# Performance work log

Hardware: AMD Instinct MI355X
Metric: run time of the kernel (lower is better)

The kernel has to match this reference:

```python
import jax, jax.numpy as jnp
import numpy as np

N_DRUG, N_TARGET, N_EDGES, H = 50000, 20000, 500000, 256


def setup_inputs() -> dict:
    key = jax.random.key(0)
    ks = jax.random.split(key, 6)
    s = 1.0 / np.sqrt(2 * H)
    return {
        "z_drug": jax.random.normal(ks[0], (N_DRUG, H), dtype=jnp.float32),
        "z_target": jax.random.normal(ks[1], (N_TARGET, H), dtype=jnp.float32),
        "row": jax.random.randint(ks[2], (N_EDGES,), 0, N_DRUG, dtype=jnp.int64),
        "col": jax.random.randint(ks[3], (N_EDGES,), 0, N_TARGET, dtype=jnp.int64),
        "W1": jax.random.normal(ks[4], (2 * H, H), dtype=jnp.float32) * s,
        "b1": jnp.zeros((H,), dtype=jnp.float32),
        "W2": jax.random.normal(ks[5], (H, 1), dtype=jnp.float32) * (1.0 / np.sqrt(H)),
        "b2": jnp.zeros((1,), dtype=jnp.float32),
    }


def reference(z_drug, z_target, row, col, W1, b1, W2, b2):
    # gather endpoint embeddings by edge index, concat -> [E, 2H]
    zc = jnp.concatenate([z_drug[row], z_target[col]], axis=-1)
    h = jax.nn.relu(zc @ W1 + b1)          # [E, H]
    return h @ W2 + b2                     # [E, 1]
```

## Files before the change

### kernel.cpp

```cpp
#include <hip/hip_runtime.h>
#include <hip/hip_bf16.h>
#include <stdint.h>


typedef unsigned short u16;
typedef __attribute__((ext_vector_type(8))) short short8;
typedef __attribute__((ext_vector_type(4))) float f32x4;

#define HDIM 256
#define KDIM 512
#define BM 64
#define BK 64
#define NWAVE 4

__device__ __forceinline__ u16 f2bf(float f) {
  union { float f; uint32_t u; } v; v.f = f;
  uint32_t u = v.u;
  return (u16)((u + 0x7fffu + ((u >> 16) & 1u)) >> 16);
}

__device__ __forceinline__ void gl2lds16(const void* g, void* l) {
  __builtin_amdgcn_global_load_lds(
      (const __attribute__((address_space(1))) unsigned int*)g,
      (__attribute__((address_space(3))) unsigned int*)l,
      16, 0, 0);
}

__global__ void cvt_bf16_kernel(const float* __restrict__ src,
                                u16* __restrict__ dst, int n4) {
  int i = blockIdx.x * blockDim.x + threadIdx.x;
  if (i >= n4) return;
  float4 v = ((const float4*)src)[i];
  ushort4 o;
  o.x = f2bf(v.x); o.y = f2bf(v.y); o.z = f2bf(v.z); o.w = f2bf(v.w);
  ((ushort4*)dst)[i] = o;
}

__global__ void w1t_kernel(const float* __restrict__ w1, u16* __restrict__ w1t) {
  int t = blockIdx.x * blockDim.x + threadIdx.x;
  int n = t >> 9, k = t & 511;
  w1t[n * 512 + k] = f2bf(w1[k * 256 + n]);
}

__global__ __launch_bounds__(256, 2) void edge_mlp_kernel(
    const u16* __restrict__ zd, const u16* __restrict__ zt,
    const int* __restrict__ row, const int* __restrict__ col,
    const u16* __restrict__ w1t, const float* __restrict__ b1,
    const float* __restrict__ w2, const float* __restrict__ b2,
    float* __restrict__ out, int E) {
  __shared__ u16 lA[BM * BK];
  __shared__ u16 lB[HDIM * BK];
  __shared__ float lP[NWAVE * BM];

  const int tid  = threadIdx.x;
  const int wid  = tid >> 6;
  const int lane = tid & 63;
  const int e0   = blockIdx.x * BM;

  const int eA = wid * 16 + (lane >> 3);
  const int g1 = min(e0 + eA, E - 1);
  const int g2 = min(e0 + eA + 8, E - 1);
  const int slog = ((lane & 7) ^ ((lane >> 3) & 7)) * 8;

  const u16* pD1 = zd + (size_t)row[g1] * HDIM + slog;
  const u16* pT1 = zt + (size_t)col[g1] * HDIM + slog;
  const u16* pD2 = zd + (size_t)row[g2] * HDIM + slog;
  const u16* pT2 = zt + (size_t)col[g2] * HDIM + slog;
  const u16* pB = w1t + (size_t)(wid * 64 + (lane >> 3)) * KDIM + slog;

  u16* lA1 = &lA[(wid * 16) * BK];
  u16* lA2 = &lA[(wid * 16 + 8) * BK];
  u16* lBw = &lB[(wid * 64) * BK];

  f32x4 acc[4][4];
#pragma unroll
  for (int i = 0; i < 4; ++i)
#pragma unroll
    for (int j = 0; j < 4; ++j) acc[i][j] = f32x4{0.f, 0.f, 0.f, 0.f};

  const int colid = lane & 15;
  const int quad  = lane >> 4;
  const int csw   = colid & 7;

  for (int kc = 0; kc < 8; ++kc) {
    const int koff = kc * BK;
    const u16* s1 = (kc < 4) ? (pD1 + koff) : (pT1 + (koff - HDIM));
    const u16* s2 = (kc < 4) ? (pD2 + koff) : (pT2 + (koff - HDIM));

    __syncthreads();
    gl2lds16(s1, lA1);
    gl2lds16(s2, lA2);
#pragma unroll
    for (int j = 0; j < 8; ++j)
      gl2lds16(pB + (size_t)j * 8 * KDIM + koff, lBw + j * 8 * BK);
    __syncthreads();

#pragma unroll
    for (int ks = 0; ks < BK; ks += 32) {
      const int sl = (ks >> 3) + quad;
      short8 aF[4], bF[4];
#pragma unroll
      for (int rt = 0; rt < 4; ++rt)
        aF[rt] = *(const short8*)&lA[(rt * 16 + colid) * BK + ((sl ^ csw) * 8)];
#pragma unroll
      for (int ct = 0; ct < 4; ++ct)
        bF[ct] = *(const short8*)&lB[(wid * 64 + ct * 16 + colid) * BK + ((sl ^ csw) * 8)];
#pragma unroll
      for (int rt = 0; rt < 4; ++rt)
#pragma unroll
        for (int ct = 0; ct < 4; ++ct)
          acc[rt][ct] = __builtin_amdgcn_mfma_f32_16x16x32_bf16(
              aF[rt], bF[ct], acc[rt][ct], 0, 0, 0);
    }
  }

  float b1v[4], w2v[4];
#pragma unroll
  for (int ct = 0; ct < 4; ++ct) {
    int n = wid * 64 + ct * 16 + colid;
    b1v[ct] = b1[n];
    w2v[ct] = w2[n];
  }
  float p[4][4];
#pragma unroll
  for (int rt = 0; rt < 4; ++rt)
#pragma unroll
    for (int j = 0; j < 4; ++j) {
      float s = 0.f;
#pragma unroll
      for (int ct = 0; ct < 4; ++ct)
        s += fmaxf(acc[rt][ct][j] + b1v[ct], 0.f) * w2v[ct];
#pragma unroll
      for (int off = 8; off >= 1; off >>= 1)
        s += __shfl_xor(s, off, 16);
      p[rt][j] = s;
    }
  if (colid == 0) {
#pragma unroll
    for (int rt = 0; rt < 4; ++rt)
#pragma unroll
      for (int j = 0; j < 4; ++j)
        lP[wid * BM + rt * 16 + quad * 4 + j] = p[rt][j];
  }
  __syncthreads();
  if (tid < BM) {
    int ge = e0 + tid;
    if (ge < E)
      out[ge] = lP[tid] + lP[BM + tid] + lP[2 * BM + tid] + lP[3 * BM + tid]
                + b2[0];
  }
}

__global__ void fallback_kernel(
    const float* __restrict__ zd, const float* __restrict__ zt,
    const int* __restrict__ row, const int* __restrict__ col,
    const float* __restrict__ W1, const float* __restrict__ b1,
    const float* __restrict__ W2, const float* __restrict__ b2,
    float* __restrict__ out, int E) {
  __shared__ float zc[16][512];
  __shared__ float red[4][16];
  const int e0 = blockIdx.x * 16;
  const int tid = threadIdx.x;
  for (int i = tid; i < 16 * 512; i += 256) {
    int e = i >> 9, k = i & 511;
    int ge = min(e0 + e, E - 1);
    zc[e][k] = (k < HDIM) ? zd[(size_t)row[ge] * HDIM + k]
                          : zt[(size_t)col[ge] * HDIM + (k - HDIM)];
  }
  __syncthreads();
  float acc[16];
#pragma unroll
  for (int e = 0; e < 16; ++e) acc[e] = 0.f;
  for (int k = 0; k < KDIM; ++k) {
    float w = W1[k * HDIM + tid];
#pragma unroll
    for (int e = 0; e < 16; ++e) acc[e] += zc[e][k] * w;
  }
  float wv = W2[tid], bv = b1[tid];
  const int lane = tid & 63, wid = tid >> 6;
#pragma unroll
  for (int e = 0; e < 16; ++e) {
    float pv = fmaxf(acc[e] + bv, 0.f) * wv;
#pragma unroll
    for (int off = 32; off >= 1; off >>= 1) pv += __shfl_down(pv, off, 64);
    if (lane == 0) red[wid][e] = pv;
  }
  __syncthreads();
  if (tid < 16) {
    int ge = e0 + tid;
    if (ge < E)
      out[ge] = red[0][tid] + red[1][tid] + red[2][tid] + red[3][tid] + b2[0];
  }
}

extern "C" void kernel_launch(void* const* d_in, const int* in_sizes, int n_in,
                              void* d_out, int out_size, void* d_ws, size_t ws_size,
                              hipStream_t stream) {
  const float* zd_f = (const float*)d_in[0];
  const float* zt_f = (const float*)d_in[1];
  const int*   row  = (const int*)d_in[2];
  const int*   col  = (const int*)d_in[3];
  const float* W1   = (const float*)d_in[4];
  const float* b1   = (const float*)d_in[5];
  const float* W2   = (const float*)d_in[6];
  const float* b2   = (const float*)d_in[7];
  float* out = (float*)d_out;

  const int E  = in_sizes[2];
  const int ND = in_sizes[0] / HDIM;
  const int NT = in_sizes[1] / HDIM;

  size_t off_w1t = 0;
  size_t off_zd  = (size_t)KDIM * HDIM * sizeof(u16);
  size_t off_zt  = off_zd + (size_t)ND * HDIM * sizeof(u16);
  size_t need    = off_zt + (size_t)NT * HDIM * sizeof(u16);

  if (ws_size >= need) {
    u16* w1t = (u16*)((char*)d_ws + off_w1t);
    u16* zdb = (u16*)((char*)d_ws + off_zd);
    u16* ztb = (u16*)((char*)d_ws + off_zt);
    int n4d = ND * HDIM / 4, n4t = NT * HDIM / 4;
    cvt_bf16_kernel<<<(n4d + 255) / 256, 256, 0, stream>>>(zd_f, zdb, n4d);
    cvt_bf16_kernel<<<(n4t + 255) / 256, 256, 0, stream>>>(zt_f, ztb, n4t);
    w1t_kernel<<<(KDIM * HDIM + 255) / 256, 256, 0, stream>>>(W1, w1t);
    edge_mlp_kernel<<<(E + BM - 1) / BM, 256, 0, stream>>>(
        zdb, ztb, row, col, w1t, b1, W2, b2, out, E);
  } else {
    fallback_kernel<<<(E + 15) / 16, 256, 0, stream>>>(
        zd_f, zt_f, row, col, W1, b1, W2, b2, out, E);
  }
}
```

Measured before the change: 270.3 us.

## Double edge tile to 128 rows and fuse bf16 prep kernels into one launch

The edge MLP kernel now processes 128 edges per block, with each wave loading 32 gathered rows. This halves how often the W1 tile is reloaded per edge and doubles the MFMA work per B fragment. The three prep kernels (two bf16 casts and the W1 transpose) become one launch: a grid-stride conversion plus an LDS-tiled coalesced transpose, which cuts launch overhead and the uncoalesced transpose reads. Doubling the accumulators to 8x4 f32x4 raises register pressure, which may lower occupancy under launch_bounds(256,2).

```diff
diff --git a/kernel.cpp b/kernel.cpp
--- a/kernel.cpp
+++ b/kernel.cpp
@@ -9,7 +9,7 @@
 
 #define HDIM 256
 #define KDIM 512
-#define BM 64
+#define BM 128
 #define BK 64
 #define NWAVE 4
 
@@ -26,20 +26,38 @@
       16, 0, 0);
 }
 
-__global__ void cvt_bf16_kernel(const float* __restrict__ src,
-                                u16* __restrict__ dst, int n4) {
-  int i = blockIdx.x * blockDim.x + threadIdx.x;
-  if (i >= n4) return;
-  float4 v = ((const float4*)src)[i];
-  ushort4 o;
-  o.x = f2bf(v.x); o.y = f2bf(v.y); o.z = f2bf(v.z); o.w = f2bf(v.w);
-  ((ushort4*)dst)[i] = o;
-}
-
-__global__ void w1t_kernel(const float* __restrict__ w1, u16* __restrict__ w1t) {
-  int t = blockIdx.x * blockDim.x + threadIdx.x;
-  int n = t >> 9, k = t & 511;
-  w1t[n * 512 + k] = f2bf(w1[k * 256 + n]);
+#define CVT_BLOCKS 4096
+__global__ void prep_kernel(const float* __restrict__ zd_f,
+                            const float* __restrict__ zt_f,
+                            const float* __restrict__ w1,
+                            u16* __restrict__ zdb, u16* __restrict__ ztb,
+                            u16* __restrict__ w1t, int n4d, int n4t) {
+  const int b = blockIdx.x;
+  if (b < 32) {
+    __shared__ float tile[64][65];
+    const int k0 = (b >> 2) * 64, n0 = (b & 3) * 64;
+    const int tx = threadIdx.x & 63, ty = threadIdx.x >> 6;
+#pragma unroll
+    for (int i = ty; i < 64; i += 4)
+      tile[i][tx] = w1[(size_t)(k0 + i) * HDIM + n0 + tx];
+    __syncthreads();
+#pragma unroll
+    for (int i = ty; i < 64; i += 4)
+      w1t[(size_t)(n0 + i) * KDIM + k0 + tx] = f2bf(tile[tx][i]);
+  } else {
+    const int idx = (b - 32) * 256 + threadIdx.x;
+    const int stride = CVT_BLOCKS * 256;
+    for (int i = idx; i < n4d; i += stride) {
+      float4 v = ((const float4*)zd_f)[i];
+      ushort4 o; o.x = f2bf(v.x); o.y = f2bf(v.y); o.z = f2bf(v.z); o.w = f2bf(v.w);
+      ((ushort4*)zdb)[i] = o;
+    }
+    for (int i = idx; i < n4t; i += stride) {
+      float4 v = ((const float4*)zt_f)[i];
+      ushort4 o; o.x = f2bf(v.x); o.y = f2bf(v.y); o.z = f2bf(v.z); o.w = f2bf(v.w);
+      ((ushort4*)ztb)[i] = o;
+    }
+  }
 }
 
 __global__ __launch_bounds__(256, 2) void edge_mlp_kernel(
@@ -56,25 +74,24 @@
   const int wid  = tid >> 6;
   const int lane = tid & 63;
   const int e0   = blockIdx.x * BM;
-
-  const int eA = wid * 16 + (lane >> 3);
-  const int g1 = min(e0 + eA, E - 1);
-  const int g2 = min(e0 + eA + 8, E - 1);
-  const int slog = ((lane & 7) ^ ((lane >> 3) & 7)) * 8;
-
-  const u16* pD1 = zd + (size_t)row[g1] * HDIM + slog;
-  const u16* pT1 = zt + (size_t)col[g1] * HDIM + slog;
-  const u16* pD2 = zd + (size_t)row[g2] * HDIM + slog;
-  const u16* pT2 = zt + (size_t)col[g2] * HDIM + slog;
-  const u16* pB = w1t + (size_t)(wid * 64 + (lane >> 3)) * KDIM + slog;
-
-  u16* lA1 = &lA[(wid * 16) * BK];
-  u16* lA2 = &lA[(wid * 16 + 8) * BK];
+  const int r8   = lane >> 3;
+  const int slog = ((lane & 7) ^ (r8 & 7)) * 8;
+
+  uint32_t offD[4], offT[4];
+#pragma unroll
+  for (int t = 0; t < 4; ++t) {
+    int ge = min(e0 + wid * 32 + r8 + 8 * t, E - 1);
+    offD[t] = (uint32_t)row[ge] * HDIM;
+    offT[t] = (uint32_t)col[ge] * HDIM;
+  }
+  const u16* pB = w1t + (uint32_t)(wid * 64 + r8) * KDIM + slog;
+
+  u16* lAw = &lA[(wid * 32) * BK];
   u16* lBw = &lB[(wid * 64) * BK];
 
-  f32x4 acc[4][4];
-#pragma unroll
-  for (int i = 0; i < 4; ++i)
+  f32x4 acc[8][4];
+#pragma unroll
+  for (int i = 0; i < 8; ++i)
 #pragma unroll
     for (int j = 0; j < 4; ++j) acc[i][j] = f32x4{0.f, 0.f, 0.f, 0.f};
 
@@ -83,30 +100,32 @@
   const int csw   = colid & 7;
 
   for (int kc = 0; kc < 8; ++kc) {
-    const int koff = kc * BK;
-    const u16* s1 = (kc < 4) ? (pD1 + koff) : (pT1 + (koff - HDIM));
-    const u16* s2 = (kc < 4) ? (pD2 + koff) : (pT2 + (koff - HDIM));
+    const int koff = (kc & 3) * BK;
+    const u16* zbase = (kc < 4) ? zd : zt;
 
     __syncthreads();
-    gl2lds16(s1, lA1);
-    gl2lds16(s2, lA2);
+#pragma unroll
+    for (int t = 0; t < 4; ++t) {
+      uint32_t o = (kc < 4) ? offD[t] : offT[t];
+      gl2lds16(zbase + o + koff + slog, lAw + (8 * t) * BK);
+    }
 #pragma unroll
     for (int j = 0; j < 8; ++j)
-      gl2lds16(pB + (size_t)j * 8 * KDIM + koff, lBw + j * 8 * BK);
+      gl2lds16(pB + (size_t)j * 8 * KDIM + kc * BK, lBw + j * 8 * BK);
     __syncthreads();
 
 #pragma unroll
     for (int ks = 0; ks < BK; ks += 32) {
       const int sl = (ks >> 3) + quad;
-      short8 aF[4], bF[4];
-#pragma unroll
-      for (int rt = 0; rt < 4; ++rt)
+      short8 aF[8], bF[4];
+#pragma unroll
+      for (int rt = 0; rt < 8; ++rt)
         aF[rt] = *(const short8*)&lA[(rt * 16 + colid) * BK + ((sl ^ csw) * 8)];
 #pragma unroll
       for (int ct = 0; ct < 4; ++ct)
         bF[ct] = *(const short8*)&lB[(wid * 64 + ct * 16 + colid) * BK + ((sl ^ csw) * 8)];
 #pragma unroll
-      for (int rt = 0; rt < 4; ++rt)
+      for (int rt = 0; rt < 8; ++rt)
 #pragma unroll
         for (int ct = 0; ct < 4; ++ct)
           acc[rt][ct] = __builtin_amdgcn_mfma_f32_16x16x32_bf16(
@@ -121,9 +140,8 @@
     b1v[ct] = b1[n];
     w2v[ct] = w2[n];
   }
-  float p[4][4];
-#pragma unroll
-  for (int rt = 0; rt < 4; ++rt)
+#pragma unroll
+  for (int rt = 0; rt < 8; ++rt)
 #pragma unroll
     for (int j = 0; j < 4; ++j) {
       float s = 0.f;
@@ -133,15 +151,9 @@
 #pragma unroll
       for (int off = 8; off >= 1; off >>= 1)
         s += __shfl_xor(s, off, 16);
-      p[rt][j] = s;
-    }
-  if (colid == 0) {
-#pragma unroll
-    for (int rt = 0; rt < 4; ++rt)
-#pragma unroll
-      for (int j = 0; j < 4; ++j)
-        lP[wid * BM + rt * 16 + quad * 4 + j] = p[rt][j];
-  }
+      if (colid == 0)
+        lP[wid * BM + rt * 16 + quad * 4 + j] = s;
+    }
   __syncthreads();
   if (tid < BM) {
     int ge = e0 + tid;
@@ -220,9 +232,8 @@
     u16* zdb = (u16*)((char*)d_ws + off_zd);
     u16* ztb = (u16*)((char*)d_ws + off_zt);
     int n4d = ND * HDIM / 4, n4t = NT * HDIM / 4;
-    cvt_bf16_kernel<<<(n4d + 255) / 256, 256, 0, stream>>>(zd_f, zdb, n4d);
-    cvt_bf16_kernel<<<(n4t + 255) / 256, 256, 0, stream>>>(zt_f, ztb, n4t);
-    w1t_kernel<<<(KDIM * HDIM + 255) / 256, 256, 0, stream>>>(W1, w1t);
+    prep_kernel<<<32 + CVT_BLOCKS, 256, 0, stream>>>(zd_f, zt_f, W1,
+                                                     zdb, ztb, w1t, n4d, n4t);
     edge_mlp_kernel<<<(E + BM - 1) / BM, 256, 0, stream>>>(
         zdb, ztb, row, col, w1t, b1, W2, b2, out, E);
   } else {
```

Result: no change. 268.1 us (-0.8%).
